# Optimization experiments

Hardware: AMD Instinct MI355X
Metric: run time of the kernel (lower is better)

## Reference

```python
import jax, jax.numpy as jnp
import numpy as np

NUM_HEADS = 16


def setup_inputs() -> dict:
    key = jax.random.key(0)
    ks = jax.random.split(key, 5)
    B, S, D = 4, 2048, 1024
    scale = 1.0 / np.sqrt(D)
    return {
        "x": jax.random.normal(ks[0], (B, S, D), dtype=jnp.float32),
        "Wq": jax.random.normal(ks[1], (D, D), dtype=jnp.float32) * scale,
        "Wk": jax.random.normal(ks[2], (D, D), dtype=jnp.float32) * scale,
        "Wv": jax.random.normal(ks[3], (D, D), dtype=jnp.float32) * scale,
        "Wo": jax.random.normal(ks[4], (D, D), dtype=jnp.float32) * scale,
    }


def reference(x, Wq, Wk, Wv, Wo):
    # x: [B, S, D]; weights are torch Linear weights [out, in], applied as x @ W.T
    B, S, D = x.shape
    H = NUM_HEADS
    dk = D // H

    def split_heads(t):  # [B,S,D] -> [B,H,S,dk]
        return t.reshape(B, S, H, dk).transpose(0, 2, 1, 3)

    q = split_heads(x @ Wq.T)
    k = split_heads(x @ Wk.T)
    v = split_heads(x @ Wv.T)

    scores = jnp.einsum("bhqd,bhkd->bhqk", q, k) / jnp.sqrt(jnp.float32(dk))
    causal = jnp.triu(jnp.ones((S, S), dtype=bool), k=1)  # True above diagonal
    scores = jnp.where(causal, -jnp.inf, scores)
    probs = jax.nn.softmax(scores, axis=-1)

    out = jnp.einsum("bhqk,bhkd->bhqd", probs, v)  # [B,H,S,dk]
    out = out.transpose(0, 2, 1, 3).reshape(B, S, D)
    return out @ Wo.T
```

## Files before the change

kernel.cpp:

```cpp
#include <hip/hip_runtime.h>

typedef __bf16 bf16_t;
using bf16x8 = __attribute__((ext_vector_type(8))) __bf16;
using bf16x4 = __attribute__((ext_vector_type(4))) __bf16;
using f32x4  = __attribute__((ext_vector_type(4))) float;

#define B_   4
#define S_   2048
#define D_   1024
#define H_   16
#define DK_  64
#define SQKV 3072

__device__ __forceinline__ void gload_lds16(const void* g, void* l) {
  __builtin_amdgcn_global_load_lds((const __attribute__((address_space(1))) void*)g,
                                   (__attribute__((address_space(3))) void*)l, 16, 0, 0);
}

__device__ __forceinline__ float fast_exp2(float x) {
#if __has_builtin(__builtin_amdgcn_exp2f)
  return __builtin_amdgcn_exp2f(x);
#else
  return __expf(x * 0.69314718f);
#endif
}

__global__ void cast_f32_to_bf16(const float* __restrict__ in, bf16_t* __restrict__ out,
                                 int n4, float scale) {
  int i = blockIdx.x * 256 + threadIdx.x;
  if (i >= n4) return;
  float4 v = reinterpret_cast<const float4*>(in)[i];
  bf16x4 o;
  o[0] = (bf16_t)(v.x * scale); o[1] = (bf16_t)(v.y * scale);
  o[2] = (bf16_t)(v.z * scale); o[3] = (bf16_t)(v.w * scale);
  reinterpret_cast<bf16x4*>(out)[i] = o;
}

template <typename OutT>
__global__ void gemm_bt(const bf16_t* __restrict__ A, const bf16_t* __restrict__ Bm,
                        OutT* __restrict__ C, int M, int N, int K) {
  __shared__ alignas(16) char As[16384];
  __shared__ alignas(16) char Bs[16384];
  const int tid  = threadIdx.x;
  const int wid  = tid >> 6, lane = tid & 63;
  const int g    = lane >> 4, l15 = lane & 15;

  int nwg = gridDim.x * gridDim.y;
  int bid = blockIdx.y * gridDim.x + blockIdx.x;
  int sb  = ((nwg & 7) == 0) ? ((bid & 7) * (nwg >> 3) + (bid >> 3)) : bid;
  int bx  = sb % gridDim.x, by = sb / gridDim.x;

  const long row0 = (long)by * 128, col0 = (long)bx * 128;
  const int wr = (wid >> 1) * 64, wc = (wid & 1) * 64;
  f32x4 acc[4][4] = {};

  for (int k0 = 0; k0 < K; k0 += 64) {
    __syncthreads();
#pragma unroll
    for (int i = 0; i < 4; ++i) {
      int L = i * 256 + tid;
      int r = L >> 3, s = L & 7;
      int sc = s ^ (r & 7);
      const bf16_t* ga = A  + (row0 + r) * (long)K + k0 + sc * 8;
      const bf16_t* gb = Bm + (col0 + r) * (long)K + k0 + sc * 8;
      gload_lds16(ga, As + (i * 256 + wid * 64) * 16);
      gload_lds16(gb, Bs + (i * 256 + wid * 64) * 16);
    }
    __syncthreads();
#pragma unroll
    for (int kk = 0; kk < 2; ++kk) {
      bf16x8 af[4], bfr[4];
#pragma unroll
      for (int m = 0; m < 4; ++m) {
        int r = wr + m * 16 + l15;
        int s = (kk * 4 + g) ^ (r & 7);
        af[m] = *reinterpret_cast<const bf16x8*>(As + r * 128 + s * 16);
      }
#pragma unroll
      for (int n = 0; n < 4; ++n) {
        int r = wc + n * 16 + l15;
        int s = (kk * 4 + g) ^ (r & 7);
        bfr[n] = *reinterpret_cast<const bf16x8*>(Bs + r * 128 + s * 16);
      }
#pragma unroll
      for (int m = 0; m < 4; ++m)
#pragma unroll
        for (int n = 0; n < 4; ++n)
          acc[m][n] = __builtin_amdgcn_mfma_f32_16x16x32_bf16(af[m], bfr[n], acc[m][n], 0, 0, 0);
    }
  }
#pragma unroll
  for (int m = 0; m < 4; ++m)
#pragma unroll
    for (int n = 0; n < 4; ++n)
#pragma unroll
      for (int j = 0; j < 4; ++j) {
        long r = row0 + wr + m * 16 + g * 4 + j;
        long c = col0 + wc + n * 16 + l15;
        C[r * (long)N + c] = (OutT)acc[m][n][j];
      }
}

__global__ void vtrans_kernel(const bf16_t* __restrict__ qkv, bf16_t* __restrict__ VT) {
  __shared__ bf16_t t[64 * 65];
  const int tid = threadIdx.x;
  const int s0 = blockIdx.x * 64;
  const int bh = blockIdx.y, b = bh >> 4, h = bh & 15;
  {
    int sl = tid >> 2, dc = tid & 3;
    const bf16_t* src = qkv + ((long)(b * S_ + s0 + sl)) * SQKV + 2 * D_ + h * DK_ + dc * 16;
    bf16x8 v0 = *reinterpret_cast<const bf16x8*>(src);
    bf16x8 v1 = *reinterpret_cast<const bf16x8*>(src + 8);
#pragma unroll
    for (int e = 0; e < 8; ++e) t[sl * 65 + dc * 16 + e] = v0[e];
#pragma unroll
    for (int e = 0; e < 8; ++e) t[sl * 65 + dc * 16 + 8 + e] = v1[e];
  }
  __syncthreads();
  {
    int d = tid >> 2, sc = tid & 3;
    bf16x8 o0, o1;
#pragma unroll
    for (int e = 0; e < 8; ++e) {
      int p  = sc * 16 + e;
      int kv = ((p >> 5) << 5) + (((p >> 2) & 1) << 4) + (((p >> 3) & 3) << 2) + (p & 3);
      o0[e] = t[kv * 65 + d];
    }
#pragma unroll
    for (int e = 0; e < 8; ++e) {
      int p  = sc * 16 + 8 + e;
      int kv = ((p >> 5) << 5) + (((p >> 2) & 1) << 4) + (((p >> 3) & 3) << 2) + (p & 3);
      o1[e] = t[kv * 65 + d];
    }
    bf16_t* dst = VT + ((long)(bh * 64 + d)) * S_ + s0 + sc * 16;
    *reinterpret_cast<bf16x8*>(dst) = o0;
    *reinterpret_cast<bf16x8*>(dst + 8) = o1;
  }
}

__global__ __launch_bounds__(256, 5)
void attn_kernel(const bf16_t* __restrict__ qkv, const bf16_t* __restrict__ VT,
                 bf16_t* __restrict__ Ob) {
  __shared__ alignas(16) char ldsK[2][8192];
  __shared__ alignas(16) char ldsV[2][8192];
  const int tid = threadIdx.x;
  const int w   = tid >> 6, lane = tid & 63;
  const int g   = lane >> 4, l15 = lane & 15;

  int bid = blockIdx.y * 32 + blockIdx.x;
  int sb  = (bid & 7) * 256 + (bid >> 3);
  const int qt = 31 - (sb & 31);
  const int bh = sb >> 5;
  const int b  = bh >> 4, h = bh & 15;
  const long rowbase = (long)b * S_;

  bf16x8 qf[2];
  {
    const bf16_t* qp = qkv + (rowbase + qt * 64 + w * 16 + l15) * SQKV + h * DK_ + g * 8;
    qf[0] = *reinterpret_cast<const bf16x8*>(qp);
    qf[1] = *reinterpret_cast<const bf16x8*>(qp + 32);
  }
  float m_q = -1e30f, ssum = 0.f;
  f32x4 oacc[4] = {};

  const bf16_t* kbase = qkv + rowbase * SQKV + D_ + h * DK_;
  const bf16_t* vbase = VT + (long)bh * 64 * S_;

  auto stageK = [&](int kvt, int buf) {
#pragma unroll
    for (int i = 0; i < 2; ++i) {
      int L = i * 256 + tid;
      int r = L >> 3, s = L & 7;
      int sc = s ^ (r & 7);
      gload_lds16(kbase + (long)(kvt * 64 + r) * SQKV + sc * 8,
                  ldsK[buf] + L * 16);
    }
  };
  auto stageV = [&](int kvt, int buf) {
#pragma unroll
    for (int i = 0; i < 2; ++i) {
      int L = i * 256 + tid;
      int r = L >> 3, s = L & 7;
      int sc = s ^ (r & 7);
      gload_lds16(vbase + (long)r * S_ + kvt * 64 + sc * 8,
                  ldsV[buf] + L * 16);
    }
  };

  stageK(0, 0); stageV(0, 0);

  const int ql = w * 16 + l15;
  const int gj = g * 4;

  for (int kvt = 0; kvt <= qt; ++kvt) {
    const int cur = kvt & 1;
    asm volatile("s_waitcnt vmcnt(0)" ::: "memory");
    __builtin_amdgcn_s_barrier();
    if (kvt < qt) { stageK(kvt + 1, cur ^ 1); stageV(kvt + 1, cur ^ 1); }

    f32x4 sv[4];
    __builtin_amdgcn_s_setprio(1);
#pragma unroll
    for (int c = 0; c < 4; ++c) {
      f32x4 a = {};
#pragma unroll
      for (int kk = 0; kk < 2; ++kk) {
        int r = c * 16 + l15;
        int s = (kk * 4 + g) ^ (l15 & 7);
        bf16x8 kf = *reinterpret_cast<const bf16x8*>(ldsK[cur] + r * 128 + s * 16);
        a = __builtin_amdgcn_mfma_f32_16x16x32_bf16(kf, qf[kk], a, 0, 0, 0);
      }
      sv[c] = a;
    }
    __builtin_amdgcn_s_setprio(0);

    if (kvt == qt) {
#pragma unroll
      for (int c = 0; c < 4; ++c)
#pragma unroll
        for (int j = 0; j < 4; ++j)
          if ((c * 16 + gj + j) > ql) sv[c][j] = -1e30f;
    }

    float mxi = sv[0][0];
#pragma unroll
    for (int c = 0; c < 4; ++c)
#pragma unroll
      for (int j = 0; j < 4; ++j) mxi = fmaxf(mxi, sv[c][j]);
    if (__any(mxi > m_q + 8.0f)) {
      float mx = fmaxf(mxi, __shfl_xor(mxi, 16));
      mx = fmaxf(mx, __shfl_xor(mx, 32));
      float mn = fmaxf(m_q, mx);
      float al = fast_exp2(m_q - mn);
      m_q = mn;
      ssum *= al;
#pragma unroll
      for (int dc = 0; dc < 4; ++dc)
#pragma unroll
        for (int j = 0; j < 4; ++j) oacc[dc][j] *= al;
    }

    bf16x8 pb[2];
#pragma unroll
    for (int ks = 0; ks < 2; ++ks)
#pragma unroll
      for (int half = 0; half < 2; ++half) {
        int c = ks * 2 + half;
#pragma unroll
        for (int j = 0; j < 4; ++j) {
          float p = fast_exp2(sv[c][j] - m_q);
          ssum += p;
          pb[ks][half * 4 + j] = (bf16_t)p;
        }
      }

    __builtin_amdgcn_s_setprio(1);
#pragma unroll
    for (int ks = 0; ks < 2; ++ks)
#pragma unroll
      for (int dc = 0; dc < 4; ++dc) {
        int r = dc * 16 + l15;
        int s = (ks * 4 + g) ^ (l15 & 7);
        bf16x8 vf = *reinterpret_cast<const bf16x8*>(ldsV[cur] + r * 128 + s * 16);
        oacc[dc] = __builtin_amdgcn_mfma_f32_16x16x32_bf16(vf, pb[ks], oacc[dc], 0, 0, 0);
      }
    __builtin_amdgcn_s_setprio(0);
  }

  ssum += __shfl_xor(ssum, 16);
  ssum += __shfl_xor(ssum, 32);
  float inv = 1.0f / ssum;
  long r = rowbase + qt * 64 + w * 16 + l15;
#pragma unroll
  for (int dc = 0; dc < 4; ++dc) {
    bf16x4 o;
#pragma unroll
    for (int j = 0; j < 4; ++j) o[j] = (bf16_t)(oacc[dc][j] * inv);
    *reinterpret_cast<bf16x4*>(&Ob[r * D_ + h * DK_ + dc * 16 + gj]) = o;
  }
}

extern "C" void kernel_launch(void* const* d_in, const int* in_sizes, int n_in,
                              void* d_out, int out_size, void* d_ws, size_t ws_size,
                              hipStream_t stream) {
  const float* x  = (const float*)d_in[0];
  const float* Wq = (const float*)d_in[1];
  const float* Wk = (const float*)d_in[2];
  const float* Wv = (const float*)d_in[3];
  const float* Wo = (const float*)d_in[4];
  float* out = (float*)d_out;

  char* ws = (char*)d_ws;
  bf16_t* xb  = (bf16_t*)(ws);
  bf16_t* Wc  = (bf16_t*)(ws + 16777216);
  bf16_t* Wob = (bf16_t*)(ws + 23068672);
  bf16_t* QKV = (bf16_t*)(ws + 25165824);
  bf16_t* Ob  = (bf16_t*)(ws + 75497472);
  bf16_t* VT  = xb;

  const float QSCALE = 0.18033688f;

  cast_f32_to_bf16<<<8192, 256, 0, stream>>>(x,  xb,            2097152, 1.0f);
  cast_f32_to_bf16<<<1024, 256, 0, stream>>>(Wq, Wc,             262144, QSCALE);
  cast_f32_to_bf16<<<1024, 256, 0, stream>>>(Wk, Wc + 1048576,   262144, 1.0f);
  cast_f32_to_bf16<<<1024, 256, 0, stream>>>(Wv, Wc + 2097152,   262144, 1.0f);
  cast_f32_to_bf16<<<1024, 256, 0, stream>>>(Wo, Wob,            262144, 1.0f);

  gemm_bt<bf16_t><<<dim3(24, 64), 256, 0, stream>>>(xb, Wc, QKV, 8192, 3072, 1024);
  vtrans_kernel<<<dim3(32, 64), 256, 0, stream>>>(QKV, VT);
  attn_kernel<<<dim3(32, 64), 256, 0, stream>>>(QKV, VT, Ob);
  gemm_bt<float><<<dim3(8, 64), 256, 0, stream>>>(Ob, Wob, out, 8192, 1024, 1024);
}
```

Baseline: 254.8 us.

## Process two 64-row query tiles per attention block to reuse K/V tiles

Each attention workgroup now handles 128 query rows, as two 64-row halves held in separate register sets, instead of 64. Every K/V tile staged in LDS feeds twice the MFMA work, which halves the K/V global traffic and the number of barriers per query row. Each half keeps its own online-softmax state and causal mask, and the final tile masks out the first half entirely. The cost is doubled accumulator registers (launch bounds lowered to 4 waves per SIMD), half as many workgroups, and some wasted MFMA work on the fully masked first half in the last KV tile.

```diff
diff --git a/kernel.cpp b/kernel.cpp
--- a/kernel.cpp
+++ b/kernel.cpp
@@ -138,7 +138,7 @@
   }
 }
 
-__global__ __launch_bounds__(256, 5)
+__global__ __launch_bounds__(256, 4)
 void attn_kernel(const bf16_t* __restrict__ qkv, const bf16_t* __restrict__ VT,
                  bf16_t* __restrict__ Ob) {
   __shared__ alignas(16) char ldsK[2][8192];
@@ -147,21 +147,24 @@
   const int w   = tid >> 6, lane = tid & 63;
   const int g   = lane >> 4, l15 = lane & 15;
 
-  int bid = blockIdx.y * 32 + blockIdx.x;
-  int sb  = (bid & 7) * 256 + (bid >> 3);
-  const int qt = 31 - (sb & 31);
-  const int bh = sb >> 5;
+  int bid = blockIdx.y * 16 + blockIdx.x;
+  int sb  = (bid & 7) * 128 + (bid >> 3);
+  const int qt = 15 - (sb & 15);
+  const int bh = sb >> 4;
   const int b  = bh >> 4, h = bh & 15;
   const long rowbase = (long)b * S_;
 
-  bf16x8 qf[2];
+  bf16x8 qf0[2], qf1[2];
   {
-    const bf16_t* qp = qkv + (rowbase + qt * 64 + w * 16 + l15) * SQKV + h * DK_ + g * 8;
-    qf[0] = *reinterpret_cast<const bf16x8*>(qp);
-    qf[1] = *reinterpret_cast<const bf16x8*>(qp + 32);
-  }
-  float m_q = -1e30f, ssum = 0.f;
-  f32x4 oacc[4] = {};
+    const bf16_t* qp0 = qkv + (rowbase + qt * 128 + w * 16 + l15) * SQKV + h * DK_ + g * 8;
+    qf0[0] = *reinterpret_cast<const bf16x8*>(qp0);
+    qf0[1] = *reinterpret_cast<const bf16x8*>(qp0 + 32);
+    const bf16_t* qp1 = qp0 + 64 * SQKV;
+    qf1[0] = *reinterpret_cast<const bf16x8*>(qp1);
+    qf1[1] = *reinterpret_cast<const bf16x8*>(qp1 + 32);
+  }
+  float m0 = -1e30f, m1 = -1e30f, s0 = 0.f, s1 = 0.f;
+  f32x4 o0[4] = {}, o1[4] = {};
 
   const bf16_t* kbase = qkv + rowbase * SQKV + D_ + h * DK_;
   const bf16_t* vbase = VT + (long)bh * 64 * S_;
@@ -187,60 +190,83 @@
     }
   };
 
+  const int last = 2 * qt + 1;
   stageK(0, 0); stageV(0, 0);
 
-  const int ql = w * 16 + l15;
+  const int qlocal = w * 16 + l15;
   const int gj = g * 4;
 
-  for (int kvt = 0; kvt <= qt; ++kvt) {
+  for (int kvt = 0; kvt <= last; ++kvt) {
     const int cur = kvt & 1;
     asm volatile("s_waitcnt vmcnt(0)" ::: "memory");
     __builtin_amdgcn_s_barrier();
-    if (kvt < qt) { stageK(kvt + 1, cur ^ 1); stageV(kvt + 1, cur ^ 1); }
-
-    f32x4 sv[4];
+    if (kvt < last) { stageK(kvt + 1, cur ^ 1); stageV(kvt + 1, cur ^ 1); }
+
+    f32x4 sv0[4], sv1[4];
     __builtin_amdgcn_s_setprio(1);
 #pragma unroll
     for (int c = 0; c < 4; ++c) {
-      f32x4 a = {};
+      f32x4 a0 = {}, a1 = {};
 #pragma unroll
       for (int kk = 0; kk < 2; ++kk) {
         int r = c * 16 + l15;
         int s = (kk * 4 + g) ^ (l15 & 7);
         bf16x8 kf = *reinterpret_cast<const bf16x8*>(ldsK[cur] + r * 128 + s * 16);
-        a = __builtin_amdgcn_mfma_f32_16x16x32_bf16(kf, qf[kk], a, 0, 0, 0);
-      }
-      sv[c] = a;
+        a0 = __builtin_amdgcn_mfma_f32_16x16x32_bf16(kf, qf0[kk], a0, 0, 0, 0);
+        a1 = __builtin_amdgcn_mfma_f32_16x16x32_bf16(kf, qf1[kk], a1, 0, 0, 0);
+      }
+      sv0[c] = a0; sv1[c] = a1;
     }
     __builtin_amdgcn_s_setprio(0);
 
-    if (kvt == qt) {
+    if (kvt == 2 * qt) {
 #pragma unroll
       for (int c = 0; c < 4; ++c)
 #pragma unroll
         for (int j = 0; j < 4; ++j)
-          if ((c * 16 + gj + j) > ql) sv[c][j] = -1e30f;
-    }
-
-    float mxi = sv[0][0];
+          if ((c * 16 + gj + j) > qlocal) sv0[c][j] = -1e30f;
+    } else if (kvt == last) {
+#pragma unroll
+      for (int c = 0; c < 4; ++c)
+#pragma unroll
+        for (int j = 0; j < 4; ++j) {
+          sv0[c][j] = -1e30f;
+          if ((c * 16 + gj + j) > qlocal) sv1[c][j] = -1e30f;
+        }
+    }
+
+    float mx0 = sv0[0][0], mx1 = sv1[0][0];
 #pragma unroll
     for (int c = 0; c < 4; ++c)
 #pragma unroll
-      for (int j = 0; j < 4; ++j) mxi = fmaxf(mxi, sv[c][j]);
-    if (__any(mxi > m_q + 8.0f)) {
-      float mx = fmaxf(mxi, __shfl_xor(mxi, 16));
+      for (int j = 0; j < 4; ++j) {
+        mx0 = fmaxf(mx0, sv0[c][j]);
+        mx1 = fmaxf(mx1, sv1[c][j]);
+      }
+    if (__any(mx0 > m0 + 8.0f)) {
+      float mx = fmaxf(mx0, __shfl_xor(mx0, 16));
       mx = fmaxf(mx, __shfl_xor(mx, 32));
-      float mn = fmaxf(m_q, mx);
-      float al = fast_exp2(m_q - mn);
-      m_q = mn;
-      ssum *= al;
+      float mn = fmaxf(m0, mx);
+      float al = fast_exp2(m0 - mn);
+      m0 = mn; s0 *= al;
 #pragma unroll
       for (int dc = 0; dc < 4; ++dc)
 #pragma unroll
-        for (int j = 0; j < 4; ++j) oacc[dc][j] *= al;
-    }
-
-    bf16x8 pb[2];
+        for (int j = 0; j < 4; ++j) o0[dc][j] *= al;
+    }
+    if (__any(mx1 > m1 + 8.0f)) {
+      float mx = fmaxf(mx1, __shfl_xor(mx1, 16));
+      mx = fmaxf(mx, __shfl_xor(mx, 32));
+      float mn = fmaxf(m1, mx);
+      float al = fast_exp2(m1 - mn);
+      m1 = mn; s1 *= al;
+#pragma unroll
+      for (int dc = 0; dc < 4; ++dc)
+#pragma unroll
+        for (int j = 0; j < 4; ++j) o1[dc][j] *= al;
+    }
+
+    bf16x8 pb0[2], pb1[2];
 #pragma unroll
     for (int ks = 0; ks < 2; ++ks)
 #pragma unroll
@@ -248,9 +274,11 @@
         int c = ks * 2 + half;
 #pragma unroll
         for (int j = 0; j < 4; ++j) {
-          float p = fast_exp2(sv[c][j] - m_q);
-          ssum += p;
-          pb[ks][half * 4 + j] = (bf16_t)p;
+          float p0 = fast_exp2(sv0[c][j] - m0);
+          float p1 = fast_exp2(sv1[c][j] - m1);
+          s0 += p0; s1 += p1;
+          pb0[ks][half * 4 + j] = (bf16_t)p0;
+          pb1[ks][half * 4 + j] = (bf16_t)p1;
         }
       }
 
@@ -262,21 +290,26 @@
         int r = dc * 16 + l15;
         int s = (ks * 4 + g) ^ (l15 & 7);
         bf16x8 vf = *reinterpret_cast<const bf16x8*>(ldsV[cur] + r * 128 + s * 16);
-        oacc[dc] = __builtin_amdgcn_mfma_f32_16x16x32_bf16(vf, pb[ks], oacc[dc], 0, 0, 0);
+        o0[dc] = __builtin_amdgcn_mfma_f32_16x16x32_bf16(vf, pb0[ks], o0[dc], 0, 0, 0);
+        o1[dc] = __builtin_amdgcn_mfma_f32_16x16x32_bf16(vf, pb1[ks], o1[dc], 0, 0, 0);
       }
     __builtin_amdgcn_s_setprio(0);
   }
 
-  ssum += __shfl_xor(ssum, 16);
-  ssum += __shfl_xor(ssum, 32);
-  float inv = 1.0f / ssum;
-  long r = rowbase + qt * 64 + w * 16 + l15;
+  s0 += __shfl_xor(s0, 16); s0 += __shfl_xor(s0, 32);
+  s1 += __shfl_xor(s1, 16); s1 += __shfl_xor(s1, 32);
+  float inv0 = 1.0f / s0, inv1 = 1.0f / s1;
+  long r0 = rowbase + qt * 128 + w * 16 + l15;
 #pragma unroll
   for (int dc = 0; dc < 4; ++dc) {
-    bf16x4 o;
-#pragma unroll
-    for (int j = 0; j < 4; ++j) o[j] = (bf16_t)(oacc[dc][j] * inv);
-    *reinterpret_cast<bf16x4*>(&Ob[r * D_ + h * DK_ + dc * 16 + gj]) = o;
+    bf16x4 oa, ob;
+#pragma unroll
+    for (int j = 0; j < 4; ++j) {
+      oa[j] = (bf16_t)(o0[dc][j] * inv0);
+      ob[j] = (bf16_t)(o1[dc][j] * inv1);
+    }
+    *reinterpret_cast<bf16x4*>(&Ob[r0 * D_ + h * DK_ + dc * 16 + gj]) = oa;
+    *reinterpret_cast<bf16x4*>(&Ob[(r0 + 64) * D_ + h * DK_ + dc * 16 + gj]) = ob;
   }
 }
 
@@ -308,6 +341,6 @@
 
   gemm_bt<bf16_t><<<dim3(24, 64), 256, 0, stream>>>(xb, Wc, QKV, 8192, 3072, 1024);
   vtrans_kernel<<<dim3(32, 64), 256, 0, stream>>>(QKV, VT);
-  attn_kernel<<<dim3(32, 64), 256, 0, stream>>>(QKV, VT, Ob);
+  attn_kernel<<<dim3(16, 64), 256, 0, stream>>>(QKV, VT, Ob);
   gemm_bt<float><<<dim3(8, 64), 256, 0, stream>>>(Ob, Wob, out, 8192, 1024, 1024);
 }
```

After: 270.5 us. 1.06x slower.
